# Performance work log

Hardware: AMD Instinct MI355X
Metric: run time of the kernel (lower is better)

## Reference

```python
import jax, jax.numpy as jnp
import numpy as np

N = 50000      # nodes
E = 800000     # edges
F_IN = 64      # n_features
H = 128        # graph_hidden_layers
LAT = 128      # latent_size
DH = 1024      # dense_hidden_layers
G = 256        # num graphs in batch
EPS = 1e-5


def setup_inputs() -> dict:
    key = jax.random.key(0)
    ks = jax.random.split(key, 32)
    def rn(k, shape, scale=0.05):
        return jax.random.normal(k, shape, dtype=jnp.float32) * scale
    inp = {
        "x": jax.random.normal(ks[0], (N, F_IN), dtype=jnp.float32),
        "origin": jax.random.normal(ks[1], (G, 3), dtype=jnp.float32),
        "direction": jax.random.normal(ks[2], (G, 3), dtype=jnp.float32),
        "edge_index": jax.random.randint(ks[3], (2, E), 0, N, dtype=jnp.int32),
        "batch": jnp.sort(jax.random.randint(ks[4], (N,), 0, G, dtype=jnp.int32)),
        # GCNConv weights
        "W1": rn(ks[5], (F_IN, H)), "b1": jnp.zeros((H,), jnp.float32),
        "W2": rn(ks[6], (H, H)),    "b2": jnp.zeros((H,), jnp.float32),
        "W3": rn(ks[7], (H, LAT)), "b3": jnp.zeros((LAT,), jnp.float32),
        # BatchNorm affine params
        "g1": jnp.ones((H,), jnp.float32),   "be1": jnp.zeros((H,), jnp.float32),
        "g2": jnp.ones((H,), jnp.float32),   "be2": jnp.zeros((H,), jnp.float32),
        "g3": jnp.ones((LAT,), jnp.float32), "be3": jnp.zeros((LAT,), jnp.float32),
        # Dense head: (LAT+6)->DH, then n_dense_layers=2 of DH->DH, then DH->3
        "Wd0": rn(ks[8], (LAT + 6, DH)), "bd0": jnp.zeros((DH,), jnp.float32),
        "Wd1": rn(ks[9], (DH, DH)),      "bd1": jnp.zeros((DH,), jnp.float32),
        "Wd2": rn(ks[10], (DH, DH)),     "bd2": jnp.zeros((DH,), jnp.float32),
        "Wout": rn(ks[11], (DH, 3)),     "bout": jnp.zeros((3,), jnp.float32),
    }
    return inp


def _gcn_conv(x, W, b, src, dst, deg_inv_sqrt):
    """PyG GCNConv with self-loops: D^{-1/2} (A+I) D^{-1/2} x W + b."""
    xW = x @ W  # [N, out]
    norm = deg_inv_sqrt[src] * deg_inv_sqrt[dst]  # [E]
    msg = xW[src] * norm[:, None]                 # gather + scale
    agg = jax.ops.segment_sum(msg, dst, num_segments=N)
    agg = agg + xW * (deg_inv_sqrt * deg_inv_sqrt)[:, None]  # self-loop term
    return agg + b


def _batchnorm(x, gamma, beta):
    m = jnp.mean(x, axis=0)
    v = jnp.mean(jnp.square(x - m), axis=0)
    return (x - m) * jax.lax.rsqrt(v + EPS) * gamma + beta


def reference(x, origin, direction, edge_index, batch,
              W1, b1, W2, b2, W3, b3,
              g1, be1, g2, be2, g3, be3,
              Wd0, bd0, Wd1, bd1, Wd2, bd2, Wout, bout):
    src, dst = edge_index[0], edge_index[1]
    # degree with self-loops (in-degree at dst, matching gcn_norm)
    deg = jax.ops.segment_sum(jnp.ones((E,), jnp.float32), dst, num_segments=N) + 1.0
    deg_inv_sqrt = jax.lax.rsqrt(deg)

    h = jax.nn.relu(_batchnorm(_gcn_conv(x, W1, b1, src, dst, deg_inv_sqrt), g1, be1))
    h = jax.nn.relu(_batchnorm(_gcn_conv(h, W2, b2, src, dst, deg_inv_sqrt), g2, be2))
    h = _batchnorm(_gcn_conv(h, W3, b3, src, dst, deg_inv_sqrt), g3, be3)

    # global mean pool over graphs
    sums = jax.ops.segment_sum(h, batch, num_segments=G)
    cnt = jax.ops.segment_sum(jnp.ones((N,), jnp.float32), batch, num_segments=G)
    pooled = sums / jnp.maximum(cnt, 1.0)[:, None]  # [G, LAT]

    z = jnp.concatenate([pooled, origin, direction], axis=1)  # [G, LAT+6]
    z = jax.nn.relu(z @ Wd0 + bd0)
    z = jax.nn.relu(z @ Wd1 + bd1)
    z = jax.nn.relu(z @ Wd2 + bd2)
    return z @ Wout + bout  # [G, 3]
```

## Files before the change

### kernel.cpp

```cpp
#include <hip/hip_runtime.h>

#define HC 128
#define FIN 64
#define DHID 1024
#define ZK 134
#define ZKP 160

typedef __attribute__((ext_vector_type(8))) short short8;
typedef __attribute__((ext_vector_type(8))) __bf16 bf16x8;
typedef __attribute__((ext_vector_type(4))) float f32x4;
typedef __attribute__((ext_vector_type(8))) unsigned short u16x8;
typedef __attribute__((ext_vector_type(4))) unsigned short u16x4;

union FragU { short8 s; bf16x8 b; u16x8 u; };

__device__ inline unsigned short rne_bf16(float x) {
    union { float f; unsigned u; } v; v.f = x;
    unsigned u = v.u;
    unsigned r = (u + 0x7fffu + ((u >> 16) & 1u)) >> 16;
    return (unsigned short)r;
}
__device__ inline float bf16_to_f(unsigned short h) {
    union { unsigned u; float f; } v; v.u = ((unsigned)h) << 16;
    return v.f;
}

__global__ void k_deg_rank(const int* __restrict__ dst, int* __restrict__ cnt,
                           int* __restrict__ rank, int E) {
    int i = blockIdx.x * blockDim.x + threadIdx.x;
    if (i < E) rank[i] = atomicAdd(&cnt[dst[i]], 1);
}

__global__ void k_xtobf(const float* __restrict__ x, const float* __restrict__ dinv,
                        unsigned short* __restrict__ xb, int n4) {
    int i = blockIdx.x * blockDim.x + threadIdx.x;
    if (i >= n4) return;
    float d = dinv[i / (FIN / 4)];
    float4 v = ((const float4*)x)[i];
    u16x4 o;
    o[0] = rne_bf16(v.x * d); o[1] = rne_bf16(v.y * d);
    o[2] = rne_bf16(v.z * d); o[3] = rne_bf16(v.w * d);
    ((u16x4*)xb)[i] = o;
}

__global__ void k_scan1(const int* __restrict__ cnt, int* __restrict__ part,
                        int* __restrict__ bsum, float* __restrict__ dinv, int N) {
    __shared__ int sh[256];
    int t = threadIdx.x, i = blockIdx.x * 256 + t;
    int v = (i < N) ? cnt[i] : 0;
    if (i < N) dinv[i] = rsqrtf((float)v + 1.0f);
    sh[t] = v; __syncthreads();
    #pragma unroll
    for (int off = 1; off < 256; off <<= 1) {
        int tv = (t >= off) ? sh[t - off] : 0;
        __syncthreads();
        sh[t] += tv;
        __syncthreads();
    }
    if (i < N) part[i] = sh[t] - v;
    if (t == 255) bsum[blockIdx.x] = sh[255];
}

__global__ void k_scan2(int* __restrict__ bsum, int nb) {
    __shared__ int sh[256];
    int t = threadIdx.x;
    int v = (t < nb) ? bsum[t] : 0;
    sh[t] = v; __syncthreads();
    #pragma unroll
    for (int off = 1; off < 256; off <<= 1) {
        int tv = (t >= off) ? sh[t - off] : 0;
        __syncthreads();
        sh[t] += tv;
        __syncthreads();
    }
    if (t < nb) bsum[t] = sh[t] - v;
}

__global__ void k_scan3(const int* __restrict__ part, const int* __restrict__ bsum,
                        int* __restrict__ row_start, int N) {
    int i = blockIdx.x * 256 + threadIdx.x;
    if (i < N) row_start[i] = part[i] + bsum[blockIdx.x];
}

__global__ void k_scatter3(const int* __restrict__ src, const int* __restrict__ dst,
                           const int* __restrict__ rank, const int* __restrict__ row_start,
                           int* __restrict__ csr, int E) {
    int e = blockIdx.x * blockDim.x + threadIdx.x;
    if (e >= E) return;
    int d = dst[e];
    csr[row_start[d] + rank[e]] = src[e];
}

template <int RF> struct BVec;
template <> struct BVec<64>  { using T = u16x4; static const int VPL = 4; };
template <> struct BVec<128> { using T = u16x8; static const int VPL = 8; };

template <int RF>
__global__ __launch_bounds__(256) void k_gather3(const unsigned short* __restrict__ T,
                                                 const int* __restrict__ csr,
                                                 const int* __restrict__ row_start,
                                                 const int* __restrict__ cnt,
                                                 const float* __restrict__ dinv,
                                                 unsigned short* __restrict__ agg, int N) {
    using vec = typename BVec<RF>::T;
    constexpr int VPL = BVec<RF>::VPL;
    int tid = threadIdx.x;
    int node = blockIdx.x * 16 + (tid >> 4);
    int q = tid & 15;
    if (node >= N) return;
    int beg = row_start[node];
    int end = beg + cnt[node];
    float d = dinv[node];
    vec sv = ((const vec*)(T + (size_t)node * RF))[q];
    float acc[VPL];
    #pragma unroll
    for (int i = 0; i < VPL; ++i) acc[i] = bf16_to_f(sv[i]);
    int j = beg;
    for (; j + 8 <= end; j += 8) {
        int e0 = csr[j], e1 = csr[j+1], e2 = csr[j+2], e3 = csr[j+3];
        int e4 = csr[j+4], e5 = csr[j+5], e6 = csr[j+6], e7 = csr[j+7];
        vec v0 = ((const vec*)(T + (size_t)e0 * RF))[q];
        vec v1 = ((const vec*)(T + (size_t)e1 * RF))[q];
        vec v2 = ((const vec*)(T + (size_t)e2 * RF))[q];
        vec v3 = ((const vec*)(T + (size_t)e3 * RF))[q];
        vec v4 = ((const vec*)(T + (size_t)e4 * RF))[q];
        vec v5 = ((const vec*)(T + (size_t)e5 * RF))[q];
        vec v6 = ((const vec*)(T + (size_t)e6 * RF))[q];
        vec v7 = ((const vec*)(T + (size_t)e7 * RF))[q];
        #pragma unroll
        for (int i = 0; i < VPL; ++i) {
            acc[i] += (bf16_to_f(v0[i]) + bf16_to_f(v1[i]))
                    + (bf16_to_f(v2[i]) + bf16_to_f(v3[i]))
                    + (bf16_to_f(v4[i]) + bf16_to_f(v5[i]))
                    + (bf16_to_f(v6[i]) + bf16_to_f(v7[i]));
        }
    }
    for (; j + 2 <= end; j += 2) {
        int e0 = csr[j], e1 = csr[j + 1];
        vec v0 = ((const vec*)(T + (size_t)e0 * RF))[q];
        vec v1 = ((const vec*)(T + (size_t)e1 * RF))[q];
        #pragma unroll
        for (int i = 0; i < VPL; ++i)
            acc[i] += bf16_to_f(v0[i]) + bf16_to_f(v1[i]);
    }
    if (j < end) {
        int e0 = csr[j];
        vec v0 = ((const vec*)(T + (size_t)e0 * RF))[q];
        #pragma unroll
        for (int i = 0; i < VPL; ++i) acc[i] += bf16_to_f(v0[i]);
    }
    vec o;
    #pragma unroll
    for (int i = 0; i < VPL; ++i) o[i] = rne_bf16(acc[i] * d);
    ((vec*)(agg + (size_t)node * RF))[q] = o;
}

__global__ __launch_bounds__(256) void k_bn_reduce3(const unsigned short* __restrict__ x,
                                                    float* __restrict__ stat, int N) {
    int cg = threadIdx.x & 15;
    int rr = threadIdx.x >> 4;
    int rpb = (N + gridDim.x - 1) / gridDim.x;
    int r0 = blockIdx.x * rpb;
    int r1 = min(N, r0 + rpb);
    float s0=0.f,s1=0.f,s2=0.f,s3=0.f,s4=0.f,s5=0.f,s6=0.f,s7=0.f;
    float q0=0.f,q1=0.f,q2=0.f,q3=0.f,q4=0.f,q5=0.f,q6=0.f,q7=0.f;
    for (int r = r0 + rr; r < r1; r += 16) {
        u16x8 v = *(const u16x8*)(x + (size_t)r * HC + cg * 8);
        float f;
        f = bf16_to_f(v[0]); s0 += f; q0 += f * f;
        f = bf16_to_f(v[1]); s1 += f; q1 += f * f;
        f = bf16_to_f(v[2]); s2 += f; q2 += f * f;
        f = bf16_to_f(v[3]); s3 += f; q3 += f * f;
        f = bf16_to_f(v[4]); s4 += f; q4 += f * f;
        f = bf16_to_f(v[5]); s5 += f; q5 += f * f;
        f = bf16_to_f(v[6]); s6 += f; q6 += f * f;
        f = bf16_to_f(v[7]); s7 += f; q7 += f * f;
    }
    __shared__ float sh[16][136];
    int c0 = cg * 8;
    int tid = threadIdx.x;
    sh[rr][c0+0]=s0; sh[rr][c0+1]=s1; sh[rr][c0+2]=s2; sh[rr][c0+3]=s3;
    sh[rr][c0+4]=s4; sh[rr][c0+5]=s5; sh[rr][c0+6]=s6; sh[rr][c0+7]=s7;
    __syncthreads();
    if (tid < HC) {
        float tot = 0.f;
        #pragma unroll
        for (int r2 = 0; r2 < 16; ++r2) tot += sh[r2][tid];
        atomicAdd(&stat[tid], tot);
    }
    __syncthreads();
    sh[rr][c0+0]=q0; sh[rr][c0+1]=q1; sh[rr][c0+2]=q2; sh[rr][c0+3]=q3;
    sh[rr][c0+4]=q4; sh[rr][c0+5]=q5; sh[rr][c0+6]=q6; sh[rr][c0+7]=q7;
    __syncthreads();
    if (tid < HC) {
        float tot = 0.f;
        #pragma unroll
        for (int r2 = 0; r2 < 16; ++r2) tot += sh[r2][tid];
        atomicAdd(&stat[HC + tid], tot);
    }
}

__global__ void k_bn_apply3(unsigned short* __restrict__ t, const float* __restrict__ stat,
                            const float* __restrict__ gam, const float* __restrict__ bet,
                            float invN, int total8) {
    int i = blockIdx.x * blockDim.x + threadIdx.x;
    if (i >= total8) return;
    int k0 = (i * 8) & (HC - 1);
    u16x8 v = ((const u16x8*)t)[i];
    u16x8 o;
    #pragma unroll
    for (int j = 0; j < 8; ++j) {
        int k = k0 + j;
        float m = stat[k] * invN;
        float var = stat[HC + k] * invN - m * m;
        float istd = rsqrtf(var + 1e-5f);
        float sc = gam[k] * istd;
        float sh = bet[k] - m * sc;
        o[j] = rne_bf16(fmaxf(bf16_to_f(v[j]) * sc + sh, 0.f));
    }
    ((u16x8*)t)[i] = o;
}

__global__ void k_pool(const unsigned short* __restrict__ h, const int* __restrict__ batch,
                       const float* __restrict__ stat, const float* __restrict__ gam,
                       const float* __restrict__ bet, float invN,
                       float* __restrict__ pooled, float* __restrict__ cnt, int N) {
    int t = threadIdx.x;
    float m = stat[t] * invN;
    float var = stat[HC + t] * invN - m * m;
    float istd = rsqrtf(var + 1e-5f);
    float scv = gam[t] * istd;
    float shv = bet[t] - m * scv;
    int rpb = (N + gridDim.x - 1) / gridDim.x;
    int r0 = blockIdx.x * rpb;
    int r1 = min(N, r0 + rpb);
    if (r0 >= r1) return;
    int curb = batch[r0];
    float acc = 0.f; float c = 0.f;
    for (int r = r0; r < r1; ++r) {
        int b = batch[r];
        if (b != curb) {
            atomicAdd(&pooled[curb * HC + t], acc);
            if (t == 0) atomicAdd(&cnt[curb], c);
            curb = b; acc = 0.f; c = 0.f;
        }
        acc += bf16_to_f(h[(size_t)r * HC + t]) * scv + shv;
        c += 1.f;
    }
    atomicAdd(&pooled[curb * HC + t], acc);
    if (t == 0) atomicAdd(&cnt[curb], c);
}

__global__ void k_build_z(const float* __restrict__ pooled, const float* __restrict__ cnt,
                          const float* __restrict__ origin, const float* __restrict__ dir,
                          float* __restrict__ z, int G) {
    int g = blockIdx.x;
    int t = threadIdx.x;
    if (t >= ZKP) return;
    float v = 0.f;
    if (t < HC) {
        float c = fmaxf(cnt[g], 1.0f);
        v = pooled[g * HC + t] / c;
    } else if (t < HC + 3) {
        v = origin[g * 3 + (t - HC)];
    } else if (t < HC + 6) {
        v = dir[g * 3 + (t - HC - 3)];
    }
    z[g * ZKP + t] = v;
}

__global__ void k_wprep_all(const float* __restrict__ W1, const float* __restrict__ W2,
                            const float* __restrict__ W3,
                            unsigned short* __restrict__ w1h, unsigned short* __restrict__ w1l,
                            unsigned short* __restrict__ w2h, unsigned short* __restrict__ w2l,
                            unsigned short* __restrict__ w3h, unsigned short* __restrict__ w3l) {
    int i = blockIdx.x * blockDim.x + threadIdx.x;
    const float* W; unsigned short *th, *tl; int K, idx;
    if (i < FIN * HC)           { W = W1; th = w1h; tl = w1l; K = FIN; idx = i; }
    else if (i < FIN*HC + HC*HC){ W = W2; th = w2h; tl = w2l; K = HC;  idx = i - FIN*HC; }
    else if (i < FIN*HC + 2*HC*HC){ W = W3; th = w3h; tl = w3l; K = HC; idx = i - FIN*HC - HC*HC; }
    else return;
    int k = idx >> 7, n = idx & (HC - 1);
    float w = W[idx];
    unsigned short h = rne_bf16(w);
    th[n * K + k] = h;
    tl[n * K + k] = rne_bf16(w - bf16_to_f(h));
}

__global__ __launch_bounds__(256) void k_wprep2(const float* __restrict__ W,
                                                unsigned short* __restrict__ th,
                                                unsigned short* __restrict__ tl,
                                                int K, int KP, int NC) {
    __shared__ float tile[32][33];
    int kt = blockIdx.x * 32, nt = blockIdx.y * 32;
    int tx = threadIdx.x & 31, ty0 = threadIdx.x >> 5;
    #pragma unroll
    for (int i = 0; i < 4; ++i) {
        int ty = ty0 + i * 8;
        int k = kt + ty;
        float v = (k < K) ? W[(size_t)k * NC + nt + tx] : 0.f;
        tile[ty][tx] = v;
    }
    __syncthreads();
    #pragma unroll
    for (int i = 0; i < 4; ++i) {
        int ty = ty0 + i * 8;
        int n = nt + ty;
        int k = kt + tx;
        float w = tile[tx][ty];
        unsigned short h = rne_bf16(w);
        th[(size_t)n * KP + k] = h;
        tl[(size_t)n * KP + k] = rne_bf16(w - bf16_to_f(h));
    }
}

template <int KK, bool SCALE>
__global__ __launch_bounds__(512) void gemm_node2(const unsigned short* __restrict__ A,
                                                  const unsigned short* __restrict__ wth,
                                                  const unsigned short* __restrict__ wtl,
                                                  const float* __restrict__ dinv,
                                                  unsigned short* __restrict__ C, int M) {
    constexpr int KS = KK / 32;
    int tid = threadIdx.x;
    int lane = tid & 63, wid = tid >> 6;
    int rw = wid & 1, cg = wid >> 1;
    int l15 = lane & 15, l4 = lane >> 4;
    int cbase = cg * 32;

    FragU bh[2][KS], bl[2][KS];
    #pragma unroll
    for (int ct = 0; ct < 2; ++ct) {
        int n = cbase + ct * 16 + l15;
        #pragma unroll
        for (int ks = 0; ks < KS; ++ks) {
            int k = ks * 32 + l4 * 8;
            bh[ct][ks].s = *(const short8*)(wth + (size_t)n * KK + k);
            bl[ct][ks].s = *(const short8*)(wtl + (size_t)n * KK + k);
        }
    }

    #pragma unroll
    for (int rt = 0; rt < 2; ++rt) {
        int m0 = blockIdx.x * 64 + rt * 32 + rw * 16;
        if (m0 < M) {
            int arow = min(m0 + l15, M - 1);
            f32x4 zero = {0.f, 0.f, 0.f, 0.f};
            f32x4 acc[2] = {zero, zero};
            #pragma unroll
            for (int ks = 0; ks < KS; ++ks) {
                int k0 = ks * 32 + l4 * 8;
                FragU a;
                a.u = *(const u16x8*)(A + (size_t)arow * KK + k0);
                #pragma unroll
                for (int ct = 0; ct < 2; ++ct) {
                    acc[ct] = __builtin_amdgcn_mfma_f32_16x16x32_bf16(a.b, bh[ct][ks].b, acc[ct], 0, 0, 0);
                    acc[ct] = __builtin_amdgcn_mfma_f32_16x16x32_bf16(a.b, bl[ct][ks].b, acc[ct], 0, 0, 0);
                }
            }
            float dv0 = 1.f, dv1 = 1.f, dv2 = 1.f, dv3 = 1.f;
            if (SCALE) {
                int rbase = m0 + l4 * 4;
                dv0 = dinv[min(rbase + 0, M - 1)];
                dv1 = dinv[min(rbase + 1, M - 1)];
                dv2 = dinv[min(rbase + 2, M - 1)];
                dv3 = dinv[min(rbase + 3, M - 1)];
            }
            #pragma unroll
            for (int ct = 0; ct < 2; ++ct) {
                int col = cbase + ct * 16 + l15;
                #pragma unroll
                for (int r = 0; r < 4; ++r) {
                    int row = m0 + l4 * 4 + r;
                    if (row < M) {
                        float v = acc[ct][r];
                        if (SCALE) v *= (r == 0 ? dv0 : r == 1 ? dv1 : r == 2 ? dv2 : dv3);
                        C[(size_t)row * HC + col] = rne_bf16(v);
                    }
                }
            }
        }
    }
}

__global__ __launch_bounds__(256) void gemm_head_sk(const float* __restrict__ A,
                                                    const unsigned short* __restrict__ wth,
                                                    const unsigned short* __restrict__ wtl,
                                                    float* __restrict__ Cpart,
                                                    int M, int N, int K, int slice) {
    int tid = threadIdx.x;
    int lane = tid & 63, wid = tid >> 6;
    int rw = wid & 1, cw = wid >> 1;
    int l15 = lane & 15, l4 = lane >> 4;
    int m0 = blockIdx.y * 32 + rw * 16;
    int cb = blockIdx.x * 64 + cw * 32;
    int z = blockIdx.z;
    int kbeg = z * slice;
    int kend = min(K, kbeg + slice);
    if (m0 >= M) return;

    int arow = m0 + l15;
    f32x4 zero = {0.f, 0.f, 0.f, 0.f};
    f32x4 acc[2] = {zero, zero};

    for (int k0 = kbeg; k0 < kend; k0 += 32) {
        int ka = k0 + l4 * 8;
        const float4 p0 = *(const float4*)(A + (size_t)arow * K + ka);
        const float4 p1 = *(const float4*)(A + (size_t)arow * K + ka + 4);
        float av[8] = {p0.x, p0.y, p0.z, p0.w, p1.x, p1.y, p1.z, p1.w};
        FragU ah, al;
        #pragma unroll
        for (int i = 0; i < 8; ++i) {
            unsigned short h = rne_bf16(av[i]);
            ah.s[i] = (short)h;
            al.s[i] = (short)rne_bf16(av[i] - bf16_to_f(h));
        }
        #pragma unroll
        for (int ct = 0; ct < 2; ++ct) {
            int n = cb + ct * 16 + l15;
            FragU bh, bl;
            bh.s = *(const short8*)(wth + (size_t)n * K + ka);
            bl.s = *(const short8*)(wtl + (size_t)n * K + ka);
            acc[ct] = __builtin_amdgcn_mfma_f32_16x16x32_bf16(ah.b, bh.b, acc[ct], 0, 0, 0);
            acc[ct] = __builtin_amdgcn_mfma_f32_16x16x32_bf16(ah.b, bl.b, acc[ct], 0, 0, 0);
            acc[ct] = __builtin_amdgcn_mfma_f32_16x16x32_bf16(al.b, bh.b, acc[ct], 0, 0, 0);
        }
    }

    float* Cz = Cpart + (size_t)z * M * N;
    #pragma unroll
    for (int ct = 0; ct < 2; ++ct) {
        int col = cb + ct * 16 + l15;
        #pragma unroll
        for (int r = 0; r < 4; ++r) {
            int row = m0 + l4 * 4 + r;
            Cz[(size_t)row * N + col] = acc[ct][r];
        }
    }
}

__global__ void k_reduce_br(const float* __restrict__ part, const float* __restrict__ bias,
                            float* __restrict__ C, int MN, int Nmask, int NZ) {
    int i = (blockIdx.x * blockDim.x + threadIdx.x) * 4;
    if (i >= MN) return;
    float4 acc = *(const float4*)(part + i);
    for (int zz = 1; zz < NZ; ++zz) {
        float4 p = *(const float4*)(part + (size_t)zz * MN + i);
        acc.x += p.x; acc.y += p.y; acc.z += p.z; acc.w += p.w;
    }
    int n = i & Nmask;
    acc.x += bias[n]; acc.y += bias[n + 1]; acc.z += bias[n + 2]; acc.w += bias[n + 3];
    acc.x = fmaxf(acc.x, 0.f); acc.y = fmaxf(acc.y, 0.f);
    acc.z = fmaxf(acc.z, 0.f); acc.w = fmaxf(acc.w, 0.f);
    *(float4*)(C + i) = acc;
}

__global__ void k_dense_out(const float* __restrict__ z, const float* __restrict__ W,
                            const float* __restrict__ b, float* __restrict__ out, int K) {
    int g = blockIdx.x;
    const float* zr = z + (size_t)g * K;
    float a0 = 0.f, a1 = 0.f, a2 = 0.f;
    for (int k = threadIdx.x; k < K; k += blockDim.x) {
        float zv = zr[k];
        a0 += zv * W[k * 3 + 0];
        a1 += zv * W[k * 3 + 1];
        a2 += zv * W[k * 3 + 2];
    }
    __shared__ float s[768];
    s[threadIdx.x] = a0; s[256 + threadIdx.x] = a1; s[512 + threadIdx.x] = a2;
    __syncthreads();
    for (int off = 128; off > 0; off >>= 1) {
        if ((int)threadIdx.x < off) {
            s[threadIdx.x]       += s[threadIdx.x + off];
            s[256 + threadIdx.x] += s[256 + threadIdx.x + off];
            s[512 + threadIdx.x] += s[512 + threadIdx.x + off];
        }
        __syncthreads();
    }
    if (threadIdx.x == 0) {
        out[g * 3 + 0] = s[0]   + b[0];
        out[g * 3 + 1] = s[256] + b[1];
        out[g * 3 + 2] = s[512] + b[2];
    }
}

extern "C" void kernel_launch(void* const* d_in, const int* in_sizes, int n_in,
                              void* d_out, int out_size, void* d_ws, size_t ws_size,
                              hipStream_t stream) {
    const float* x         = (const float*)d_in[0];
    const float* origin    = (const float*)d_in[1];
    const float* direction = (const float*)d_in[2];
    const int*   eidx      = (const int*)d_in[3];
    const int*   batch     = (const int*)d_in[4];
    const float* W1 = (const float*)d_in[5];
    const float* W2 = (const float*)d_in[7];
    const float* W3 = (const float*)d_in[9];
    const float* g1 = (const float*)d_in[11]; const float* be1 = (const float*)d_in[12];
    const float* g2 = (const float*)d_in[13]; const float* be2 = (const float*)d_in[14];
    const float* g3 = (const float*)d_in[15]; const float* be3 = (const float*)d_in[16];
    const float* Wd0 = (const float*)d_in[17]; const float* bd0 = (const float*)d_in[18];
    const float* Wd1 = (const float*)d_in[19]; const float* bd1 = (const float*)d_in[20];
    const float* Wd2 = (const float*)d_in[21]; const float* bd2 = (const float*)d_in[22];
    const float* Wout = (const float*)d_in[23]; const float* bout = (const float*)d_in[24];
    float* out = (float*)d_out;

    const int N = in_sizes[4];
    const int E = in_sizes[3] / 2;
    const int G = in_sizes[1] / 3;
    const int* src = eidx;
    const int* dst = eidx + E;

    char* ws = (char*)d_ws;
    size_t off = 0;
    auto alloc = [&](size_t nbytes) -> void* {
        void* p = (void*)(ws + off);
        off += (nbytes + 255) & ~(size_t)255;
        return p;
    };
    float* colstats = (float*)alloc(3 * 2 * HC * 4);
    float* pooled   = (float*)alloc((size_t)G * HC * 4);
    float* cntf     = (float*)alloc((size_t)G * 4);
    int*   degcnt   = (int*)alloc((size_t)N * 4);
    const size_t zeroBytes = 3 * 2 * HC * 4 + (size_t)G * HC * 4 + 1024  + (size_t)N * 4;

    float* dinv     = (float*)alloc((size_t)N * 4);
    int*   part     = (int*)alloc((size_t)N * 4);
    int*   bsum     = (int*)alloc(256 * 4);
    int*   row_start= (int*)alloc((size_t)N * 4);
    int*   rank     = (int*)alloc((size_t)E * 4);
    int*   csr      = (int*)alloc((size_t)E * 4);
    unsigned short* xb   = (unsigned short*)alloc((size_t)N * FIN * 2);
    unsigned short* aggx = (unsigned short*)alloc((size_t)N * FIN * 2);
    unsigned short* tabA = (unsigned short*)alloc((size_t)N * HC * 2);
    unsigned short* tabB = (unsigned short*)alloc((size_t)N * HC * 2);
    unsigned short* wt1h = (unsigned short*)alloc((size_t)FIN * HC * 2);
    unsigned short* wt1l = (unsigned short*)alloc((size_t)FIN * HC * 2);
    unsigned short* wt2h = (unsigned short*)alloc((size_t)HC * HC * 2);
    unsigned short* wt2l = (unsigned short*)alloc((size_t)HC * HC * 2);
    unsigned short* wt3h = (unsigned short*)alloc((size_t)HC * HC * 2);
    unsigned short* wt3l = (unsigned short*)alloc((size_t)HC * HC * 2);
    unsigned short* wd0h = (unsigned short*)alloc((size_t)DHID * ZKP * 2);
    unsigned short* wd0l = (unsigned short*)alloc((size_t)DHID * ZKP * 2);
    unsigned short* wd1h = (unsigned short*)alloc((size_t)DHID * DHID * 2);
    unsigned short* wd1l = (unsigned short*)alloc((size_t)DHID * DHID * 2);
    unsigned short* wd2h = (unsigned short*)alloc((size_t)DHID * DHID * 2);
    unsigned short* wd2l = (unsigned short*)alloc((size_t)DHID * DHID * 2);
    float* zbuf     = (float*)alloc((size_t)G * ZKP * 4);
    float* t0       = (float*)alloc((size_t)G * DHID * 4);
    float* t1       = (float*)alloc((size_t)G * DHID * 4);
    float* kpart    = (float*)alloc((size_t)8 * G * DHID * 4);
    (void)ws_size;

    const int nScanBlk = (N + 255) / 256;
    const int gemmBlk = (N + 63) / 64;
    const int gatherBlk = (N + 15) / 16;
    const int total8 = N * HC / 8;
    const float invN = 1.0f / (float)N;

    hipMemsetAsync(colstats, 0, zeroBytes, stream);

    k_wprep_all<<<(FIN * HC + 2 * HC * HC + 255) / 256, 256, 0, stream>>>(
        W1, W2, W3, wt1h, wt1l, wt2h, wt2l, wt3h, wt3l);
    k_wprep2<<<dim3(ZKP / 32, DHID / 32), 256, 0, stream>>>(Wd0, wd0h, wd0l, ZK, ZKP, DHID);
    k_wprep2<<<dim3(DHID / 32, DHID / 32), 256, 0, stream>>>(Wd1, wd1h, wd1l, DHID, DHID, DHID);
    k_wprep2<<<dim3(DHID / 32, DHID / 32), 256, 0, stream>>>(Wd2, wd2h, wd2l, DHID, DHID, DHID);

    k_deg_rank<<<(E + 255) / 256, 256, 0, stream>>>(dst, degcnt, rank, E);
    k_scan1<<<nScanBlk, 256, 0, stream>>>(degcnt, part, bsum, dinv, N);
    k_scan2<<<1, 256, 0, stream>>>(bsum, nScanBlk);
    k_scan3<<<nScanBlk, 256, 0, stream>>>(part, bsum, row_start, N);
    k_scatter3<<<(E + 255) / 256, 256, 0, stream>>>(src, dst, rank, row_start, csr, E);

    k_xtobf<<<(N * FIN / 4 + 255) / 256, 256, 0, stream>>>(x, dinv, xb, N * FIN / 4);

    k_gather3<FIN><<<gatherBlk, 256, 0, stream>>>(xb, csr, row_start, degcnt, dinv, aggx, N);
    gemm_node2<FIN, false><<<gemmBlk, 512, 0, stream>>>(aggx, wt1h, wt1l, nullptr, tabA, N);
    k_bn_reduce3<<<256, 256, 0, stream>>>(tabA, colstats + 0 * 2 * HC, N);

    k_bn_apply3<<<(total8 + 255) / 256, 256, 0, stream>>>(tabA, colstats + 0 * 2 * HC,
                                                          g1, be1, invN, total8);
    gemm_node2<HC, true><<<gemmBlk, 512, 0, stream>>>(tabA, wt2h, wt2l, dinv, tabB, N);
    k_gather3<HC><<<gatherBlk, 256, 0, stream>>>(tabB, csr, row_start, degcnt, dinv, tabA, N);
    k_bn_reduce3<<<256, 256, 0, stream>>>(tabA, colstats + 1 * 2 * HC, N);

    k_bn_apply3<<<(total8 + 255) / 256, 256, 0, stream>>>(tabA, colstats + 1 * 2 * HC,
                                                          g2, be2, invN, total8);
    gemm_node2<HC, true><<<gemmBlk, 512, 0, stream>>>(tabA, wt3h, wt3l, dinv, tabB, N);
    k_gather3<HC><<<gatherBlk, 256, 0, stream>>>(tabB, csr, row_start, degcnt, dinv, tabA, N);
    k_bn_reduce3<<<256, 256, 0, stream>>>(tabA, colstats + 2 * 2 * HC, N);

    k_pool<<<512, HC, 0, stream>>>(tabA, batch, colstats + 2 * 2 * HC, g3, be3, invN,
                                   pooled, cntf, N);
    k_build_z<<<G, 192, 0, stream>>>(pooled, cntf, origin, direction, zbuf, G);

    const int MN = G * DHID;
    const int rblk = (MN / 4 + 255) / 256;

    gemm_head_sk<<<dim3(DHID / 64, (G + 31) / 32, 5), 256, 0, stream>>>(
        zbuf, wd0h, wd0l, kpart, G, DHID, ZKP, 32);
    k_reduce_br<<<rblk, 256, 0, stream>>>(kpart, bd0, t0, MN, DHID - 1, 5);

    gemm_head_sk<<<dim3(DHID / 64, (G + 31) / 32, 8), 256, 0, stream>>>(
        t0, wd1h, wd1l, kpart, G, DHID, DHID, 128);
    k_reduce_br<<<rblk, 256, 0, stream>>>(kpart, bd1, t1, MN, DHID - 1, 8);

    gemm_head_sk<<<dim3(DHID / 64, (G + 31) / 32, 8), 256, 0, stream>>>(
        t1, wd2h, wd2l, kpart, G, DHID, DHID, 128);
    k_reduce_br<<<rblk, 256, 0, stream>>>(kpart, bd2, t0, MN, DHID - 1, 8);

    k_dense_out<<<G, 256, 0, stream>>>(t0, Wout, bout, out, DHID);
}
```

Before: 367.7 us.

## Fuse BatchNorm statistics into GEMM/gather epilogues and merge small prep kernels

Removes the three separate BN column-reduction passes by accumulating sum and sum-of-squares in the epilogue of the producing kernel (the layer-1 GEMM and the layer-2/3 gathers), using shared-memory atomics followed by one global atomic per column per block. It also merges scan2 and scan3 into one kernel in which each block reduces the preceding block sums itself, and folds the three dense-weight prep launches into one 3D-grid launch. This saves a full re-read of the N×128 bf16 activation three times plus several launches. In exchange it adds shared-atomic contention in the hot gather and GEMM kernels, and many more global float atomics (one per column per block over about 3125 blocks), which also makes float summation order nondeterministic.

```diff
diff --git a/kernel.cpp b/kernel.cpp
--- a/kernel.cpp
+++ b/kernel.cpp
@@ -61,25 +61,20 @@
     if (t == 255) bsum[blockIdx.x] = sh[255];
 }
 
-__global__ void k_scan2(int* __restrict__ bsum, int nb) {
+__global__ void k_scan23(const int* __restrict__ part, const int* __restrict__ bsum,
+                         int* __restrict__ row_start, int nb, int N) {
     __shared__ int sh[256];
-    int t = threadIdx.x;
-    int v = (t < nb) ? bsum[t] : 0;
-    sh[t] = v; __syncthreads();
-    #pragma unroll
-    for (int off = 1; off < 256; off <<= 1) {
-        int tv = (t >= off) ? sh[t - off] : 0;
-        __syncthreads();
-        sh[t] += tv;
-        __syncthreads();
-    }
-    if (t < nb) bsum[t] = sh[t] - v;
-}
-
-__global__ void k_scan3(const int* __restrict__ part, const int* __restrict__ bsum,
-                        int* __restrict__ row_start, int N) {
-    int i = blockIdx.x * 256 + threadIdx.x;
-    if (i < N) row_start[i] = part[i] + bsum[blockIdx.x];
+    int t = threadIdx.x, b = blockIdx.x;
+    sh[t] = (t < b && t < nb) ? bsum[t] : 0;
+    __syncthreads();
+    #pragma unroll
+    for (int off = 128; off > 0; off >>= 1) {
+        if (t < off) sh[t] += sh[t + off];
+        __syncthreads();
+    }
+    int prefix = sh[0];
+    int i = b * 256 + t;
+    if (i < N) row_start[i] = part[i] + prefix;
 }
 
 __global__ void k_scatter3(const int* __restrict__ src, const int* __restrict__ dst,
@@ -95,108 +90,89 @@
 template <> struct BVec<64>  { using T = u16x4; static const int VPL = 4; };
 template <> struct BVec<128> { using T = u16x8; static const int VPL = 8; };
 
-template <int RF>
+template <int RF, bool STATS>
 __global__ __launch_bounds__(256) void k_gather3(const unsigned short* __restrict__ T,
                                                  const int* __restrict__ csr,
                                                  const int* __restrict__ row_start,
                                                  const int* __restrict__ cnt,
                                                  const float* __restrict__ dinv,
-                                                 unsigned short* __restrict__ agg, int N) {
+                                                 unsigned short* __restrict__ agg,
+                                                 float* __restrict__ stat, int N) {
     using vec = typename BVec<RF>::T;
     constexpr int VPL = BVec<RF>::VPL;
     int tid = threadIdx.x;
     int node = blockIdx.x * 16 + (tid >> 4);
     int q = tid & 15;
-    if (node >= N) return;
-    int beg = row_start[node];
-    int end = beg + cnt[node];
-    float d = dinv[node];
-    vec sv = ((const vec*)(T + (size_t)node * RF))[q];
-    float acc[VPL];
-    #pragma unroll
-    for (int i = 0; i < VPL; ++i) acc[i] = bf16_to_f(sv[i]);
-    int j = beg;
-    for (; j + 8 <= end; j += 8) {
-        int e0 = csr[j], e1 = csr[j+1], e2 = csr[j+2], e3 = csr[j+3];
-        int e4 = csr[j+4], e5 = csr[j+5], e6 = csr[j+6], e7 = csr[j+7];
-        vec v0 = ((const vec*)(T + (size_t)e0 * RF))[q];
-        vec v1 = ((const vec*)(T + (size_t)e1 * RF))[q];
-        vec v2 = ((const vec*)(T + (size_t)e2 * RF))[q];
-        vec v3 = ((const vec*)(T + (size_t)e3 * RF))[q];
-        vec v4 = ((const vec*)(T + (size_t)e4 * RF))[q];
-        vec v5 = ((const vec*)(T + (size_t)e5 * RF))[q];
-        vec v6 = ((const vec*)(T + (size_t)e6 * RF))[q];
-        vec v7 = ((const vec*)(T + (size_t)e7 * RF))[q];
+    __shared__ float ssum[HC], ssq[HC];
+    if (STATS) {
+        if (tid < HC) { ssum[tid] = 0.f; ssq[tid] = 0.f; }
+        __syncthreads();
+    }
+    bool active = node < N;
+    float acc[VPL] = {};
+    float d = 1.f;
+    if (active) {
+        int beg = row_start[node];
+        int end = beg + cnt[node];
+        d = dinv[node];
+        vec sv = ((const vec*)(T + (size_t)node * RF))[q];
         #pragma unroll
-        for (int i = 0; i < VPL; ++i) {
-            acc[i] += (bf16_to_f(v0[i]) + bf16_to_f(v1[i]))
-                    + (bf16_to_f(v2[i]) + bf16_to_f(v3[i]))
-                    + (bf16_to_f(v4[i]) + bf16_to_f(v5[i]))
-                    + (bf16_to_f(v6[i]) + bf16_to_f(v7[i]));
-        }
-    }
-    for (; j + 2 <= end; j += 2) {
-        int e0 = csr[j], e1 = csr[j + 1];
-        vec v0 = ((const vec*)(T + (size_t)e0 * RF))[q];
-        vec v1 = ((const vec*)(T + (size_t)e1 * RF))[q];
+        for (int i = 0; i < VPL; ++i) acc[i] = bf16_to_f(sv[i]);
+        int j = beg;
+        for (; j + 8 <= end; j += 8) {
+            int e0 = csr[j], e1 = csr[j+1], e2 = csr[j+2], e3 = csr[j+3];
+            int e4 = csr[j+4], e5 = csr[j+5], e6 = csr[j+6], e7 = csr[j+7];
+            vec v0 = ((const vec*)(T + (size_t)e0 * RF))[q];
+            vec v1 = ((const vec*)(T + (size_t)e1 * RF))[q];
+            vec v2 = ((const vec*)(T + (size_t)e2 * RF))[q];
+            vec v3 = ((const vec*)(T + (size_t)e3 * RF))[q];
+            vec v4 = ((const vec*)(T + (size_t)e4 * RF))[q];
+            vec v5 = ((const vec*)(T + (size_t)e5 * RF))[q];
+            vec v6 = ((const vec*)(T + (size_t)e6 * RF))[q];
+            vec v7 = ((const vec*)(T + (size_t)e7 * RF))[q];
+            #pragma unroll
+            for (int i = 0; i < VPL; ++i) {
+                acc[i] += (bf16_to_f(v0[i]) + bf16_to_f(v1[i]))
+                        + (bf16_to_f(v2[i]) + bf16_to_f(v3[i]))
+                        + (bf16_to_f(v4[i]) + bf16_to_f(v5[i]))
+                        + (bf16_to_f(v6[i]) + bf16_to_f(v7[i]));
+            }
+        }
+        for (; j + 2 <= end; j += 2) {
+            int e0 = csr[j], e1 = csr[j + 1];
+            vec v0 = ((const vec*)(T + (size_t)e0 * RF))[q];
+            vec v1 = ((const vec*)(T + (size_t)e1 * RF))[q];
+            #pragma unroll
+            for (int i = 0; i < VPL; ++i)
+                acc[i] += bf16_to_f(v0[i]) + bf16_to_f(v1[i]);
+        }
+        if (j < end) {
+            int e0 = csr[j];
+            vec v0 = ((const vec*)(T + (size_t)e0 * RF))[q];
+            #pragma unroll
+            for (int i = 0; i < VPL; ++i) acc[i] += bf16_to_f(v0[i]);
+        }
+    }
+    vec o;
+    if (active) {
         #pragma unroll
-        for (int i = 0; i < VPL; ++i)
-            acc[i] += bf16_to_f(v0[i]) + bf16_to_f(v1[i]);
-    }
-    if (j < end) {
-        int e0 = csr[j];
-        vec v0 = ((const vec*)(T + (size_t)e0 * RF))[q];
-        #pragma unroll
-        for (int i = 0; i < VPL; ++i) acc[i] += bf16_to_f(v0[i]);
-    }
-    vec o;
-    #pragma unroll
-    for (int i = 0; i < VPL; ++i) o[i] = rne_bf16(acc[i] * d);
-    ((vec*)(agg + (size_t)node * RF))[q] = o;
-}
-
-__global__ __launch_bounds__(256) void k_bn_reduce3(const unsigned short* __restrict__ x,
-                                                    float* __restrict__ stat, int N) {
-    int cg = threadIdx.x & 15;
-    int rr = threadIdx.x >> 4;
-    int rpb = (N + gridDim.x - 1) / gridDim.x;
-    int r0 = blockIdx.x * rpb;
-    int r1 = min(N, r0 + rpb);
-    float s0=0.f,s1=0.f,s2=0.f,s3=0.f,s4=0.f,s5=0.f,s6=0.f,s7=0.f;
-    float q0=0.f,q1=0.f,q2=0.f,q3=0.f,q4=0.f,q5=0.f,q6=0.f,q7=0.f;
-    for (int r = r0 + rr; r < r1; r += 16) {
-        u16x8 v = *(const u16x8*)(x + (size_t)r * HC + cg * 8);
-        float f;
-        f = bf16_to_f(v[0]); s0 += f; q0 += f * f;
-        f = bf16_to_f(v[1]); s1 += f; q1 += f * f;
-        f = bf16_to_f(v[2]); s2 += f; q2 += f * f;
-        f = bf16_to_f(v[3]); s3 += f; q3 += f * f;
-        f = bf16_to_f(v[4]); s4 += f; q4 += f * f;
-        f = bf16_to_f(v[5]); s5 += f; q5 += f * f;
-        f = bf16_to_f(v[6]); s6 += f; q6 += f * f;
-        f = bf16_to_f(v[7]); s7 += f; q7 += f * f;
-    }
-    __shared__ float sh[16][136];
-    int c0 = cg * 8;
-    int tid = threadIdx.x;
-    sh[rr][c0+0]=s0; sh[rr][c0+1]=s1; sh[rr][c0+2]=s2; sh[rr][c0+3]=s3;
-    sh[rr][c0+4]=s4; sh[rr][c0+5]=s5; sh[rr][c0+6]=s6; sh[rr][c0+7]=s7;
-    __syncthreads();
-    if (tid < HC) {
-        float tot = 0.f;
-        #pragma unroll
-        for (int r2 = 0; r2 < 16; ++r2) tot += sh[r2][tid];
-        atomicAdd(&stat[tid], tot);
-    }
-    __syncthreads();
-    sh[rr][c0+0]=q0; sh[rr][c0+1]=q1; sh[rr][c0+2]=q2; sh[rr][c0+3]=q3;
-    sh[rr][c0+4]=q4; sh[rr][c0+5]=q5; sh[rr][c0+6]=q6; sh[rr][c0+7]=q7;
-    __syncthreads();
-    if (tid < HC) {
-        float tot = 0.f;
-        #pragma unroll
-        for (int r2 = 0; r2 < 16; ++r2) tot += sh[r2][tid];
-        atomicAdd(&stat[HC + tid], tot);
+        for (int i = 0; i < VPL; ++i) o[i] = rne_bf16(acc[i] * d);
+        ((vec*)(agg + (size_t)node * RF))[q] = o;
+    }
+    if (STATS) {
+        if (active) {
+            #pragma unroll
+            for (int i = 0; i < VPL; ++i) {
+                float f = bf16_to_f(o[i]);
+                atomicAdd(&ssum[q * VPL + i], f);
+                atomicAdd(&ssq[q * VPL + i], f * f);
+            }
+        }
+        __syncthreads();
+        if (tid < HC) {
+            atomicAdd(&stat[tid], ssum[tid]);
+            atomicAdd(&stat[HC + tid], ssq[tid]);
+        }
     }
 }
 
@@ -287,10 +263,25 @@
     tl[n * K + k] = rne_bf16(w - bf16_to_f(h));
 }
 
-__global__ __launch_bounds__(256) void k_wprep2(const float* __restrict__ W,
-                                                unsigned short* __restrict__ th,
-                                                unsigned short* __restrict__ tl,
-                                                int K, int KP, int NC) {
+__global__ __launch_bounds__(256) void k_wprep2_all(const float* __restrict__ Wd0,
+                                                    const float* __restrict__ Wd1,
+                                                    const float* __restrict__ Wd2,
+                                                    unsigned short* __restrict__ d0h,
+                                                    unsigned short* __restrict__ d0l,
+                                                    unsigned short* __restrict__ d1h,
+                                                    unsigned short* __restrict__ d1l,
+                                                    unsigned short* __restrict__ d2h,
+                                                    unsigned short* __restrict__ d2l) {
+    int z = blockIdx.z;
+    const float* W; unsigned short *th, *tl; int K, KP;
+    if (z == 0) {
+        if (blockIdx.x >= ZKP / 32) return;
+        W = Wd0; th = d0h; tl = d0l; K = ZK; KP = ZKP;
+    } else if (z == 1) {
+        W = Wd1; th = d1h; tl = d1l; K = DHID; KP = DHID;
+    } else {
+        W = Wd2; th = d2h; tl = d2l; K = DHID; KP = DHID;
+    }
     __shared__ float tile[32][33];
     int kt = blockIdx.x * 32, nt = blockIdx.y * 32;
     int tx = threadIdx.x & 31, ty0 = threadIdx.x >> 5;
@@ -298,7 +289,7 @@
     for (int i = 0; i < 4; ++i) {
         int ty = ty0 + i * 8;
         int k = kt + ty;
-        float v = (k < K) ? W[(size_t)k * NC + nt + tx] : 0.f;
+        float v = (k < K) ? W[(size_t)k * DHID + nt + tx] : 0.f;
         tile[ty][tx] = v;
     }
     __syncthreads();
@@ -314,18 +305,25 @@
     }
 }
 
-template <int KK, bool SCALE>
+template <int KK, bool SCALE, bool STATS>
 __global__ __launch_bounds__(512) void gemm_node2(const unsigned short* __restrict__ A,
                                                   const unsigned short* __restrict__ wth,
                                                   const unsigned short* __restrict__ wtl,
                                                   const float* __restrict__ dinv,
-                                                  unsigned short* __restrict__ C, int M) {
+                                                  unsigned short* __restrict__ C,
+                                                  float* __restrict__ stat, int M) {
     constexpr int KS = KK / 32;
     int tid = threadIdx.x;
     int lane = tid & 63, wid = tid >> 6;
     int rw = wid & 1, cg = wid >> 1;
     int l15 = lane & 15, l4 = lane >> 4;
     int cbase = cg * 32;
+
+    __shared__ float ssum[HC], ssq[HC];
+    if (STATS) {
+        if (tid < HC) { ssum[tid] = 0.f; ssq[tid] = 0.f; }
+        __syncthreads();
+    }
 
     FragU bh[2][KS], bl[2][KS];
     #pragma unroll
@@ -338,6 +336,8 @@
             bl[ct][ks].s = *(const short8*)(wtl + (size_t)n * KK + k);
         }
     }
+
+    float ps0 = 0.f, pq0 = 0.f, ps1 = 0.f, pq1 = 0.f;
 
     #pragma unroll
     for (int rt = 0; rt < 2; ++rt) {
@@ -374,10 +374,27 @@
                     if (row < M) {
                         float v = acc[ct][r];
                         if (SCALE) v *= (r == 0 ? dv0 : r == 1 ? dv1 : r == 2 ? dv2 : dv3);
-                        C[(size_t)row * HC + col] = rne_bf16(v);
+                        unsigned short hb = rne_bf16(v);
+                        C[(size_t)row * HC + col] = hb;
+                        if (STATS) {
+                            float f = bf16_to_f(hb);
+                            if (ct == 0) { ps0 += f; pq0 += f * f; }
+                            else         { ps1 += f; pq1 += f * f; }
+                        }
                     }
                 }
             }
+        }
+    }
+
+    if (STATS) {
+        int col0 = cbase + l15, col1 = cbase + 16 + l15;
+        atomicAdd(&ssum[col0], ps0); atomicAdd(&ssq[col0], pq0);
+        atomicAdd(&ssum[col1], ps1); atomicAdd(&ssq[col1], pq1);
+        __syncthreads();
+        if (tid < HC) {
+            atomicAdd(&stat[tid], ssum[tid]);
+            atomicAdd(&stat[HC + tid], ssq[tid]);
         }
     }
 }
@@ -560,33 +577,34 @@
 
     k_wprep_all<<<(FIN * HC + 2 * HC * HC + 255) / 256, 256, 0, stream>>>(
         W1, W2, W3, wt1h, wt1l, wt2h, wt2l, wt3h, wt3l);
-    k_wprep2<<<dim3(ZKP / 32, DHID / 32), 256, 0, stream>>>(Wd0, wd0h, wd0l, ZK, ZKP, DHID);
-    k_wprep2<<<dim3(DHID / 32, DHID / 32), 256, 0, stream>>>(Wd1, wd1h, wd1l, DHID, DHID, DHID);
-    k_wprep2<<<dim3(DHID / 32, DHID / 32), 256, 0, stream>>>(Wd2, wd2h, wd2l, DHID, DHID, DHID);
+    k_wprep2_all<<<dim3(DHID / 32, DHID / 32, 3), 256, 0, stream>>>(
+        Wd0, Wd1, Wd2, wd0h, wd0l, wd1h, wd1l, wd2h, wd2l);
 
     k_deg_rank<<<(E + 255) / 256, 256, 0, stream>>>(dst, degcnt, rank, E);
     k_scan1<<<nScanBlk, 256, 0, stream>>>(degcnt, part, bsum, dinv, N);
-    k_scan2<<<1, 256, 0, stream>>>(bsum, nScanBlk);
-    k_scan3<<<nScanBlk, 256, 0, stream>>>(part, bsum, row_start, N);
+    k_scan23<<<nScanBlk, 256, 0, stream>>>(part, bsum, row_start, nScanBlk, N);
     k_scatter3<<<(E + 255) / 256, 256, 0, stream>>>(src, dst, rank, row_start, csr, E);
 
     k_xtobf<<<(N * FIN / 4 + 255) / 256, 256, 0, stream>>>(x, dinv, xb, N * FIN / 4);
 
-    k_gather3<FIN><<<gatherBlk, 256, 0, stream>>>(xb, csr, row_start, degcnt, dinv, aggx, N);
-    gemm_node2<FIN, false><<<gemmBlk, 512, 0, stream>>>(aggx, wt1h, wt1l, nullptr, tabA, N);
-    k_bn_reduce3<<<256, 256, 0, stream>>>(tabA, colstats + 0 * 2 * HC, N);
+    k_gather3<FIN, false><<<gatherBlk, 256, 0, stream>>>(xb, csr, row_start, degcnt, dinv,
+                                                         aggx, nullptr, N);
+    gemm_node2<FIN, false, true><<<gemmBlk, 512, 0, stream>>>(aggx, wt1h, wt1l, nullptr,
+                                                              tabA, colstats + 0 * 2 * HC, N);
 
     k_bn_apply3<<<(total8 + 255) / 256, 256, 0, stream>>>(tabA, colstats + 0 * 2 * HC,
                                                           g1, be1, invN, total8);
-    gemm_node2<HC, true><<<gemmBlk, 512, 0, stream>>>(tabA, wt2h, wt2l, dinv, tabB, N);
-    k_gather3<HC><<<gatherBlk, 256, 0, stream>>>(tabB, csr, row_start, degcnt, dinv, tabA, N);
-    k_bn_reduce3<<<256, 256, 0, stream>>>(tabA, colstats + 1 * 2 * HC, N);
+    gemm_node2<HC, true, false><<<gemmBlk, 512, 0, stream>>>(tabA, wt2h, wt2l, dinv,
+                                                             tabB, nullptr, N);
+    k_gather3<HC, true><<<gatherBlk, 256, 0, stream>>>(tabB, csr, row_start, degcnt, dinv,
+                                                       tabA, colstats + 1 * 2 * HC, N);
 
     k_bn_apply3<<<(total8 + 255) / 256, 256, 0, stream>>>(tabA, colstats + 1 * 2 * HC,
                                                           g2, be2, invN, total8);
-    gemm_node2<HC, true><<<gemmBlk, 512, 0, stream>>>(tabA, wt3h, wt3l, dinv, tabB, N);
-    k_gather3<HC><<<gatherBlk, 256, 0, stream>>>(tabB, csr, row_start, degcnt, dinv, tabA, N);
-    k_bn_reduce3<<<256, 256, 0, stream>>>(tabA, colstats + 2 * 2 * HC, N);
+    gemm_node2<HC, true, false><<<gemmBlk, 512, 0, stream>>>(tabA, wt3h, wt3l, dinv,
+                                                             tabB, nullptr, N);
+    k_gather3<HC, true><<<gatherBlk, 256, 0, stream>>>(tabB, csr, row_start, degcnt, dinv,
+                                                       tabA, colstats + 2 * 2 * HC, N);
 
     k_pool<<<512, HC, 0, stream>>>(tabA, batch, colstats + 2 * 2 * HC, g3, be3, invN,
                                    pooled, cntf, N);
```

Result: slower. 510.3 us (+38.8%).

## Fuse BatchNorm statistics into gather kernels and merge scan and weight-prep launches

Applied to the files above, without the earlier changes.

The layer 2 and 3 neighbour gathers now accumulate per-column sum and sum-of-squares of their bf16 outputs in a grid-stride loop. Each block reduces these through shared memory and atomically adds them into the column stats, so the separate BN reduce pass over the node table is no longer launched. The two scan kernels are merged: each block recomputes its own prefix by reducing the block sums below it. The three dense-head weight-prep launches become one 3D launch. Together these remove a full read of the 50000x128 activation table per layer and several launches, at the cost of fewer gather blocks (512 with a grid-stride loop) and float atomics whose summation order is nondeterministic.

```diff
diff --git a/kernel.cpp b/kernel.cpp
--- a/kernel.cpp
+++ b/kernel.cpp
@@ -61,25 +61,20 @@
     if (t == 255) bsum[blockIdx.x] = sh[255];
 }
 
-__global__ void k_scan2(int* __restrict__ bsum, int nb) {
+__global__ void k_scan23(const int* __restrict__ part, const int* __restrict__ bsum,
+                         int* __restrict__ row_start, int nb, int N) {
     __shared__ int sh[256];
-    int t = threadIdx.x;
-    int v = (t < nb) ? bsum[t] : 0;
-    sh[t] = v; __syncthreads();
-    #pragma unroll
-    for (int off = 1; off < 256; off <<= 1) {
-        int tv = (t >= off) ? sh[t - off] : 0;
+    int t = threadIdx.x, b = blockIdx.x;
+    sh[t] = (t < b && t < nb) ? bsum[t] : 0;
+    __syncthreads();
+    #pragma unroll
+    for (int off = 128; off > 0; off >>= 1) {
+        if (t < off) sh[t] += sh[t + off];
         __syncthreads();
-        sh[t] += tv;
-        __syncthreads();
-    }
-    if (t < nb) bsum[t] = sh[t] - v;
-}
-
-__global__ void k_scan3(const int* __restrict__ part, const int* __restrict__ bsum,
-                        int* __restrict__ row_start, int N) {
-    int i = blockIdx.x * 256 + threadIdx.x;
-    if (i < N) row_start[i] = part[i] + bsum[blockIdx.x];
+    }
+    int prefix = sh[0];
+    int i = b * 256 + t;
+    if (i < N) row_start[i] = part[i] + prefix;
 }
 
 __global__ void k_scatter3(const int* __restrict__ src, const int* __restrict__ dst,
@@ -95,64 +90,108 @@
 template <> struct BVec<64>  { using T = u16x4; static const int VPL = 4; };
 template <> struct BVec<128> { using T = u16x8; static const int VPL = 8; };
 
-template <int RF>
-__global__ __launch_bounds__(256) void k_gather3(const unsigned short* __restrict__ T,
+template <int RF, bool STATS>
+__global__ __launch_bounds__(256) void k_gather4(const unsigned short* __restrict__ T,
                                                  const int* __restrict__ csr,
                                                  const int* __restrict__ row_start,
                                                  const int* __restrict__ cnt,
                                                  const float* __restrict__ dinv,
-                                                 unsigned short* __restrict__ agg, int N) {
+                                                 unsigned short* __restrict__ agg,
+                                                 float* __restrict__ stat, int N) {
     using vec = typename BVec<RF>::T;
     constexpr int VPL = BVec<RF>::VPL;
     int tid = threadIdx.x;
-    int node = blockIdx.x * 16 + (tid >> 4);
-    int q = tid & 15;
-    if (node >= N) return;
-    int beg = row_start[node];
-    int end = beg + cnt[node];
-    float d = dinv[node];
-    vec sv = ((const vec*)(T + (size_t)node * RF))[q];
-    float acc[VPL];
-    #pragma unroll
-    for (int i = 0; i < VPL; ++i) acc[i] = bf16_to_f(sv[i]);
-    int j = beg;
-    for (; j + 8 <= end; j += 8) {
-        int e0 = csr[j], e1 = csr[j+1], e2 = csr[j+2], e3 = csr[j+3];
-        int e4 = csr[j+4], e5 = csr[j+5], e6 = csr[j+6], e7 = csr[j+7];
-        vec v0 = ((const vec*)(T + (size_t)e0 * RF))[q];
-        vec v1 = ((const vec*)(T + (size_t)e1 * RF))[q];
-        vec v2 = ((const vec*)(T + (size_t)e2 * RF))[q];
-        vec v3 = ((const vec*)(T + (size_t)e3 * RF))[q];
-        vec v4 = ((const vec*)(T + (size_t)e4 * RF))[q];
-        vec v5 = ((const vec*)(T + (size_t)e5 * RF))[q];
-        vec v6 = ((const vec*)(T + (size_t)e6 * RF))[q];
-        vec v7 = ((const vec*)(T + (size_t)e7 * RF))[q];
-        #pragma unroll
-        for (int i = 0; i < VPL; ++i) {
-            acc[i] += (bf16_to_f(v0[i]) + bf16_to_f(v1[i]))
-                    + (bf16_to_f(v2[i]) + bf16_to_f(v3[i]))
-                    + (bf16_to_f(v4[i]) + bf16_to_f(v5[i]))
-                    + (bf16_to_f(v6[i]) + bf16_to_f(v7[i]));
-        }
-    }
-    for (; j + 2 <= end; j += 2) {
-        int e0 = csr[j], e1 = csr[j + 1];
-        vec v0 = ((const vec*)(T + (size_t)e0 * RF))[q];
-        vec v1 = ((const vec*)(T + (size_t)e1 * RF))[q];
-        #pragma unroll
-        for (int i = 0; i < VPL; ++i)
-            acc[i] += bf16_to_f(v0[i]) + bf16_to_f(v1[i]);
-    }
-    if (j < end) {
-        int e0 = csr[j];
-        vec v0 = ((const vec*)(T + (size_t)e0 * RF))[q];
-        #pragma unroll
-        for (int i = 0; i < VPL; ++i) acc[i] += bf16_to_f(v0[i]);
-    }
-    vec o;
-    #pragma unroll
-    for (int i = 0; i < VPL; ++i) o[i] = rne_bf16(acc[i] * d);
-    ((vec*)(agg + (size_t)node * RF))[q] = o;
+    int slot = tid >> 4, q = tid & 15;
+    int numGrp = (N + 15) >> 4;
+    float s0=0.f,s1=0.f,s2=0.f,s3=0.f,s4=0.f,s5=0.f,s6=0.f,s7=0.f;
+    float p0=0.f,p1=0.f,p2=0.f,p3=0.f,p4=0.f,p5=0.f,p6=0.f,p7=0.f;
+
+    for (int grp = blockIdx.x; grp < numGrp; grp += gridDim.x) {
+        int node = grp * 16 + slot;
+        if (node >= N) continue;
+        int beg = row_start[node];
+        int end = beg + cnt[node];
+        float d = dinv[node];
+        vec sv = ((const vec*)(T + (size_t)node * RF))[q];
+        float acc[VPL];
+        #pragma unroll
+        for (int i = 0; i < VPL; ++i) acc[i] = bf16_to_f(sv[i]);
+        int j = beg;
+        for (; j + 8 <= end; j += 8) {
+            int e0 = csr[j], e1 = csr[j+1], e2 = csr[j+2], e3 = csr[j+3];
+            int e4 = csr[j+4], e5 = csr[j+5], e6 = csr[j+6], e7 = csr[j+7];
+            vec v0 = ((const vec*)(T + (size_t)e0 * RF))[q];
+            vec v1 = ((const vec*)(T + (size_t)e1 * RF))[q];
+            vec v2 = ((const vec*)(T + (size_t)e2 * RF))[q];
+            vec v3 = ((const vec*)(T + (size_t)e3 * RF))[q];
+            vec v4 = ((const vec*)(T + (size_t)e4 * RF))[q];
+            vec v5 = ((const vec*)(T + (size_t)e5 * RF))[q];
+            vec v6 = ((const vec*)(T + (size_t)e6 * RF))[q];
+            vec v7 = ((const vec*)(T + (size_t)e7 * RF))[q];
+            #pragma unroll
+            for (int i = 0; i < VPL; ++i) {
+                acc[i] += (bf16_to_f(v0[i]) + bf16_to_f(v1[i]))
+                        + (bf16_to_f(v2[i]) + bf16_to_f(v3[i]))
+                        + (bf16_to_f(v4[i]) + bf16_to_f(v5[i]))
+                        + (bf16_to_f(v6[i]) + bf16_to_f(v7[i]));
+            }
+        }
+        for (; j + 2 <= end; j += 2) {
+            int e0 = csr[j], e1 = csr[j + 1];
+            vec v0 = ((const vec*)(T + (size_t)e0 * RF))[q];
+            vec v1 = ((const vec*)(T + (size_t)e1 * RF))[q];
+            #pragma unroll
+            for (int i = 0; i < VPL; ++i)
+                acc[i] += bf16_to_f(v0[i]) + bf16_to_f(v1[i]);
+        }
+        if (j < end) {
+            int e0 = csr[j];
+            vec v0 = ((const vec*)(T + (size_t)e0 * RF))[q];
+            #pragma unroll
+            for (int i = 0; i < VPL; ++i) acc[i] += bf16_to_f(v0[i]);
+        }
+        vec o;
+        #pragma unroll
+        for (int i = 0; i < VPL; ++i) o[i] = rne_bf16(acc[i] * d);
+        ((vec*)(agg + (size_t)node * RF))[q] = o;
+        if (STATS) {
+            float f;
+            f = bf16_to_f(o[0]); s0 += f; p0 += f * f;
+            f = bf16_to_f(o[1]); s1 += f; p1 += f * f;
+            f = bf16_to_f(o[2]); s2 += f; p2 += f * f;
+            f = bf16_to_f(o[3]); s3 += f; p3 += f * f;
+            if (VPL == 8) {
+                f = bf16_to_f(o[4]); s4 += f; p4 += f * f;
+                f = bf16_to_f(o[5]); s5 += f; p5 += f * f;
+                f = bf16_to_f(o[6]); s6 += f; p6 += f * f;
+                f = bf16_to_f(o[7]); s7 += f; p7 += f * f;
+            }
+        }
+    }
+
+    if (STATS) {
+        __shared__ float sh[16][136];
+        int c0 = q * 8;
+        sh[slot][c0+0]=s0; sh[slot][c0+1]=s1; sh[slot][c0+2]=s2; sh[slot][c0+3]=s3;
+        sh[slot][c0+4]=s4; sh[slot][c0+5]=s5; sh[slot][c0+6]=s6; sh[slot][c0+7]=s7;
+        __syncthreads();
+        if (tid < HC) {
+            float tot = 0.f;
+            #pragma unroll
+            for (int r = 0; r < 16; ++r) tot += sh[r][tid];
+            atomicAdd(&stat[tid], tot);
+        }
+        __syncthreads();
+        sh[slot][c0+0]=p0; sh[slot][c0+1]=p1; sh[slot][c0+2]=p2; sh[slot][c0+3]=p3;
+        sh[slot][c0+4]=p4; sh[slot][c0+5]=p5; sh[slot][c0+6]=p6; sh[slot][c0+7]=p7;
+        __syncthreads();
+        if (tid < HC) {
+            float tot = 0.f;
+            #pragma unroll
+            for (int r = 0; r < 16; ++r) tot += sh[r][tid];
+            atomicAdd(&stat[HC + tid], tot);
+        }
+    }
 }
 
 __global__ __launch_bounds__(256) void k_bn_reduce3(const unsigned short* __restrict__ x,
@@ -287,10 +326,25 @@
     tl[n * K + k] = rne_bf16(w - bf16_to_f(h));
 }
 
-__global__ __launch_bounds__(256) void k_wprep2(const float* __restrict__ W,
-                                                unsigned short* __restrict__ th,
-                                                unsigned short* __restrict__ tl,
-                                                int K, int KP, int NC) {
+__global__ __launch_bounds__(256) void k_wprep2_all(const float* __restrict__ Wd0,
+                                                    const float* __restrict__ Wd1,
+                                                    const float* __restrict__ Wd2,
+                                                    unsigned short* __restrict__ d0h,
+                                                    unsigned short* __restrict__ d0l,
+                                                    unsigned short* __restrict__ d1h,
+                                                    unsigned short* __restrict__ d1l,
+                                                    unsigned short* __restrict__ d2h,
+                                                    unsigned short* __restrict__ d2l) {
+    int z = blockIdx.z;
+    const float* W; unsigned short *th, *tl; int K, KP;
+    if (z == 0) {
+        if (blockIdx.x >= ZKP / 32) return;
+        W = Wd0; th = d0h; tl = d0l; K = ZK; KP = ZKP;
+    } else if (z == 1) {
+        W = Wd1; th = d1h; tl = d1l; K = DHID; KP = DHID;
+    } else {
+        W = Wd2; th = d2h; tl = d2l; K = DHID; KP = DHID;
+    }
     __shared__ float tile[32][33];
     int kt = blockIdx.x * 32, nt = blockIdx.y * 32;
     int tx = threadIdx.x & 31, ty0 = threadIdx.x >> 5;
@@ -298,7 +352,7 @@
     for (int i = 0; i < 4; ++i) {
         int ty = ty0 + i * 8;
         int k = kt + ty;
-        float v = (k < K) ? W[(size_t)k * NC + nt + tx] : 0.f;
+        float v = (k < K) ? W[(size_t)k * DHID + nt + tx] : 0.f;
         tile[ty][tx] = v;
     }
     __syncthreads();
@@ -553,6 +607,7 @@
     const int nScanBlk = (N + 255) / 256;
     const int gemmBlk = (N + 63) / 64;
     const int gatherBlk = (N + 15) / 16;
+    const int statsGatherBlk = 512;
     const int total8 = N * HC / 8;
     const float invN = 1.0f / (float)N;
 
@@ -560,33 +615,32 @@
 
     k_wprep_all<<<(FIN * HC + 2 * HC * HC + 255) / 256, 256, 0, stream>>>(
         W1, W2, W3, wt1h, wt1l, wt2h, wt2l, wt3h, wt3l);
-    k_wprep2<<<dim3(ZKP / 32, DHID / 32), 256, 0, stream>>>(Wd0, wd0h, wd0l, ZK, ZKP, DHID);
-    k_wprep2<<<dim3(DHID / 32, DHID / 32), 256, 0, stream>>>(Wd1, wd1h, wd1l, DHID, DHID, DHID);
-    k_wprep2<<<dim3(DHID / 32, DHID / 32), 256, 0, stream>>>(Wd2, wd2h, wd2l, DHID, DHID, DHID);
+    k_wprep2_all<<<dim3(DHID / 32, DHID / 32, 3), 256, 0, stream>>>(
+        Wd0, Wd1, Wd2, wd0h, wd0l, wd1h, wd1l, wd2h, wd2l);
 
     k_deg_rank<<<(E + 255) / 256, 256, 0, stream>>>(dst, degcnt, rank, E);
     k_scan1<<<nScanBlk, 256, 0, stream>>>(degcnt, part, bsum, dinv, N);
-    k_scan2<<<1, 256, 0, stream>>>(bsum, nScanBlk);
-    k_scan3<<<nScanBlk, 256, 0, stream>>>(part, bsum, row_start, N);
+    k_scan23<<<nScanBlk, 256, 0, stream>>>(part, bsum, row_start, nScanBlk, N);
     k_scatter3<<<(E + 255) / 256, 256, 0, stream>>>(src, dst, rank, row_start, csr, E);
 
     k_xtobf<<<(N * FIN / 4 + 255) / 256, 256, 0, stream>>>(x, dinv, xb, N * FIN / 4);
 
-    k_gather3<FIN><<<gatherBlk, 256, 0, stream>>>(xb, csr, row_start, degcnt, dinv, aggx, N);
+    k_gather4<FIN, false><<<gatherBlk, 256, 0, stream>>>(xb, csr, row_start, degcnt, dinv,
+                                                         aggx, nullptr, N);
     gemm_node2<FIN, false><<<gemmBlk, 512, 0, stream>>>(aggx, wt1h, wt1l, nullptr, tabA, N);
     k_bn_reduce3<<<256, 256, 0, stream>>>(tabA, colstats + 0 * 2 * HC, N);
 
     k_bn_apply3<<<(total8 + 255) / 256, 256, 0, stream>>>(tabA, colstats + 0 * 2 * HC,
                                                           g1, be1, invN, total8);
     gemm_node2<HC, true><<<gemmBlk, 512, 0, stream>>>(tabA, wt2h, wt2l, dinv, tabB, N);
-    k_gather3<HC><<<gatherBlk, 256, 0, stream>>>(tabB, csr, row_start, degcnt, dinv, tabA, N);
-    k_bn_reduce3<<<256, 256, 0, stream>>>(tabA, colstats + 1 * 2 * HC, N);
+    k_gather4<HC, true><<<statsGatherBlk, 256, 0, stream>>>(tabB, csr, row_start, degcnt,
+                                                            dinv, tabA, colstats + 1 * 2 * HC, N);
 
     k_bn_apply3<<<(total8 + 255) / 256, 256, 0, stream>>>(tabA, colstats + 1 * 2 * HC,
                                                           g2, be2, invN, total8);
     gemm_node2<HC, true><<<gemmBlk, 512, 0, stream>>>(tabA, wt3h, wt3l, dinv, tabB, N);
-    k_gather3<HC><<<gatherBlk, 256, 0, stream>>>(tabB, csr, row_start, degcnt, dinv, tabA, N);
-    k_bn_reduce3<<<256, 256, 0, stream>>>(tabA, colstats + 2 * 2 * HC, N);
+    k_gather4<HC, true><<<statsGatherBlk, 256, 0, stream>>>(tabB, csr, row_start, degcnt,
+                                                            dinv, tabA, colstats + 2 * 2 * HC, N);
 
     k_pool<<<512, HC, 0, stream>>>(tabA, batch, colstats + 2 * 2 * HC, g3, be3, invN,
                                    pooled, cntf, N);
```

Result: no change. 368.1 us, median of 2 (+0.1%).
